# Kernel optimization log

Measured on AMD Instinct MI355X. Metric: run time of the kernel, lower is better.

## Reference

```python
import jax, jax.numpy as jnp
import numpy as np

T, N, E, F_IN, H_GNN, H_OUT, RH, G, C = 8, 10000, 160000, 128, 128, 128, 128, 32, 10


def gcn_layer(x, src, dst, W, b):
    # PyG GCNConv: h = D^-1/2 (A+I) D^-1/2 (x W) + b, self-loops added, edge weight 1
    h = x @ W  # [N, H]
    ones = jnp.ones((E,), h.dtype)
    deg = jax.ops.segment_sum(ones, dst, num_segments=N) + 1.0  # +1 for self-loop
    dinv = jax.lax.rsqrt(deg)
    coef = dinv[src] * dinv[dst]  # [E]
    agg = jax.ops.segment_sum(h[src] * coef[:, None], dst, num_segments=N)
    agg = agg + h * (dinv * dinv)[:, None]  # self-loop term
    return agg + b


def snapshot_encode(x, edge_index, batch, W1, b1, W2, b2):
    src, dst = edge_index[0], edge_index[1]
    h = jax.nn.relu(gcn_layer(x, src, dst, W1, b1))
    h = jax.nn.relu(gcn_layer(h, src, dst, W2, b2))
    sums = jax.ops.segment_sum(h, batch, num_segments=G)  # global_mean_pool
    cnts = jax.ops.segment_sum(jnp.ones((N,), h.dtype), batch, num_segments=G)
    return sums / jnp.maximum(cnts, 1.0)[:, None]  # [G, H_OUT]


def gru_layer(seq, Wih, Whh, bih, bhh):
    # seq: [T, G, in]; torch nn.GRU cell equations
    H = Whh.shape[1]

    def step(h, xt):
        gi = xt @ Wih.T + bih
        gh = h @ Whh.T + bhh
        ir, iz, inn = jnp.split(gi, 3, axis=-1)
        hr, hz, hn = jnp.split(gh, 3, axis=-1)
        r = jax.nn.sigmoid(ir + hr)
        z = jax.nn.sigmoid(iz + hz)
        n = jnp.tanh(inn + r * hn)
        h_new = (1.0 - z) * n + z * h
        return h_new, h_new

    h0 = jnp.zeros((seq.shape[1], H), seq.dtype)
    hT, outs = jax.lax.scan(step, h0, seq)
    return outs, hT


def setup_inputs() -> dict:
    key = jax.random.key(0)
    ks = jax.random.split(key, 20)
    s = 0.05
    inp = {
        "x": jax.random.normal(ks[0], (T, N, F_IN), jnp.float32),
        "edge_index": jax.random.randint(ks[1], (T, 2, E), 0, N),
        "batch": jax.random.randint(ks[2], (T, N), 0, G),
        "W1": jax.random.normal(ks[3], (F_IN, H_GNN), jnp.float32) * s,
        "b1": jnp.zeros((H_GNN,), jnp.float32),
        "W2": jax.random.normal(ks[4], (H_GNN, H_OUT), jnp.float32) * s,
        "b2": jnp.zeros((H_OUT,), jnp.float32),
        "Wih0": jax.random.normal(ks[5], (3 * RH, H_OUT), jnp.float32) * s,
        "Whh0": jax.random.normal(ks[6], (3 * RH, RH), jnp.float32) * s,
        "bih0": jnp.zeros((3 * RH,), jnp.float32),
        "bhh0": jnp.zeros((3 * RH,), jnp.float32),
        "Wih1": jax.random.normal(ks[7], (3 * RH, RH), jnp.float32) * s,
        "Whh1": jax.random.normal(ks[8], (3 * RH, RH), jnp.float32) * s,
        "bih1": jnp.zeros((3 * RH,), jnp.float32),
        "bhh1": jnp.zeros((3 * RH,), jnp.float32),
        "Wc": jax.random.normal(ks[9], (C, RH), jnp.float32) * s,
        "bc": jnp.zeros((C,), jnp.float32),
    }
    return inp


def reference(x, edge_index, batch, W1, b1, W2, b2, Wih0, Whh0, bih0, bhh0,
              Wih1, Whh1, bih1, bhh1, Wc, bc):
    # per-snapshot GNN encode, vmapped over T snapshots -> [T, G, H_OUT]
    emb = jax.vmap(snapshot_encode, in_axes=(0, 0, 0, None, None, None, None))(
        x, edge_index, batch, W1, b1, W2, b2)
    outs, _ = gru_layer(emb, Wih0, Whh0, bih0, bhh0)
    _, hT = gru_layer(outs, Wih1, Whh1, bih1, bhh1)  # h_n[-1]: last layer final state
    return hT @ Wc.T + bc  # [G, C]
```

## Files before the change

kernel.cpp:

```cpp
#include <hip/hip_runtime.h>

#define T_ 8
#define N_ 10000
#define E_ 160000
#define G_ 32
#define C_ 10
#define F_ 128

typedef _Float16 f16;
typedef _Float16 f16x2 __attribute__((ext_vector_type(2)));
typedef _Float16 f16x4 __attribute__((ext_vector_type(4)));
typedef _Float16 f16x8 __attribute__((ext_vector_type(8)));
typedef float floatx4 __attribute__((ext_vector_type(4)));

static constexpr size_t ROWS = (size_t)T_ * N_;
static constexpr int SLICE = E_ / 8;

static constexpr size_t OFF_XH    = 0;
static constexpr size_t OFF_A1    = 20480000;
static constexpr size_t OFF_H1    = 40960000;
static constexpr size_t OFF_REC   = 61440000;
static constexpr size_t OFF_CNT   = 66560000;
static constexpr size_t OFF_DINV  = 69120000;
static constexpr size_t OFF_RP    = 69440000;
static constexpr size_t OFF_CNTG  = 69760032;
static constexpr size_t OFF_BRP   = 69761056;
static constexpr size_t OFF_WP    = 69762112;
static constexpr size_t OFF_BLIST = 69827648;
static constexpr size_t OFF_GPACK = 70213184;
static constexpr size_t OFF_PART  = 70999616;

__device__ __forceinline__ float sig_fast(float x) {
  return __builtin_amdgcn_rcpf(1.0f + __builtin_amdgcn_exp2f(-1.4426950408889634f * x));
}
__device__ __forceinline__ float tanh_fast(float x) {
  return 1.0f - 2.0f * __builtin_amdgcn_rcpf(1.0f + __builtin_amdgcn_exp2f(2.8853900817779268f * x));
}

__global__ __launch_bounds__(1024) void hist_kernel(const int* __restrict__ ei,
                                                    const int* __restrict__ batch,
                                                    int* __restrict__ cnt,
                                                    int* __restrict__ cntG) {
  __shared__ int hL[N_];
  __shared__ int cL[G_];
  int b = blockIdx.x, tid = threadIdx.x;
  int t = b & 7, s = b >> 3;
  for (int i = tid; i < N_; i += 1024) hL[i] = 0;
  if (tid < G_) cL[tid] = 0;
  __syncthreads();
  const int* dstp = ei + (size_t)t * 2 * E_ + E_ + s * SLICE;
  for (int e4 = tid; e4 < SLICE / 4; e4 += 1024) {
    int4 d = *(const int4*)(dstp + e4 * 4);
    atomicAdd(&hL[d.x], 1); atomicAdd(&hL[d.y], 1);
    atomicAdd(&hL[d.z], 1); atomicAdd(&hL[d.w], 1);
  }
  if (s == 0)
    for (int n = tid; n < N_; n += 1024) atomicAdd(&cL[batch[t * N_ + n]], 1);
  __syncthreads();
  int* cp = cnt + ((size_t)t * 8 + s) * N_;
  for (int i = tid; i < N_; i += 1024) cp[i] = hL[i];
  if (s == 0 && tid < G_) cntG[t * G_ + tid] = cL[tid];
}

__global__ __launch_bounds__(1024) void scan_kernel(int* __restrict__ cnt,
                                                    int* __restrict__ rp,
                                                    float* __restrict__ dinv,
                                                    const int* __restrict__ cntG,
                                                    int* __restrict__ brp) {
  __shared__ int wsum[16];
  __shared__ int carry;
  int t = blockIdx.x, tid = threadIdx.x, lane = tid & 63, wid = tid >> 6;
  if (t == 8) {
    int v = (tid < 256) ? cntG[tid] : 0;
    for (int ofs = 1; ofs < 64; ofs <<= 1) {
      int u = __shfl_up(v, ofs);
      if (lane >= ofs) v += u;
    }
    if (lane == 63 && wid < 4) wsum[wid] = v;
    __syncthreads();
    if (tid < 256) {
      int base = 0;
      for (int w = 0; w < wid; ++w) base += wsum[w];
      if (tid == 0) brp[0] = 0;
      brp[tid + 1] = v + base;
    }
    return;
  }
  if (tid == 0) { carry = 0; rp[t * (N_ + 1)] = 0; }
  __syncthreads();
  for (int c0 = 0; c0 < N_; c0 += 1024) {
    int n = c0 + tid;
    int vs[8];
    int deg = 0;
    if (n < N_) {
#pragma unroll
      for (int s = 0; s < 8; ++s) {
        vs[s] = cnt[((size_t)t * 8 + s) * N_ + n];
        deg += vs[s];
      }
      dinv[t * N_ + n] = rsqrtf((float)deg + 1.0f);
    }
    int v = (n < N_) ? deg : 0;
    int v0 = v;
    for (int ofs = 1; ofs < 64; ofs <<= 1) {
      int u = __shfl_up(v, ofs);
      if (lane >= ofs) v += u;
    }
    if (lane == 63) wsum[wid] = v;
    __syncthreads();
    if (wid == 0) {
      int w = (lane < 16) ? wsum[lane] : 0;
      for (int ofs = 1; ofs < 16; ofs <<= 1) {
        int u = __shfl_up(w, ofs);
        if (lane >= ofs) w += u;
      }
      if (lane < 16) wsum[lane] = w;
    }
    __syncthreads();
    int base = carry + (wid ? wsum[wid - 1] : 0);
    if (n < N_) {
      rp[t * (N_ + 1) + n + 1] = base + v;
      int run = base + v - v0;
#pragma unroll
      for (int s = 0; s < 8; ++s) {
        int vv = vs[s];
        cnt[((size_t)t * 8 + s) * N_ + n] = run;
        run += vv;
      }
    }
    __syncthreads();
    if (tid == 0) carry += wsum[15];
    __syncthreads();
  }
}

__global__ __launch_bounds__(1024) void fill_kernel(const int* __restrict__ ei,
                                                    const int* __restrict__ base,
                                                    int* __restrict__ rec,
                                                    const int* __restrict__ batch,
                                                    const int* __restrict__ brp,
                                                    int* __restrict__ blist) {
  __shared__ int offL[N_];
  __shared__ int cb[G_];
  int b = blockIdx.x, tid = threadIdx.x;
  int t = b & 7, s = b >> 3;
  const int* bp = base + ((size_t)t * 8 + s) * N_;
  for (int i = tid; i < N_; i += 1024) offL[i] = bp[i];
  if (s == 0 && tid < G_) cb[tid] = brp[t * G_ + tid];
  __syncthreads();
  const int* srcp = ei + (size_t)t * 2 * E_ + s * SLICE;
  const int* dstp = srcp + E_;
  int* rt = rec + (size_t)t * E_;
  for (int e4 = tid; e4 < SLICE / 4; e4 += 1024) {
    int4 sv = *(const int4*)(srcp + e4 * 4);
    int4 dv = *(const int4*)(dstp + e4 * 4);
    int p0 = atomicAdd(&offL[dv.x], 1);
    int p1 = atomicAdd(&offL[dv.y], 1);
    int p2 = atomicAdd(&offL[dv.z], 1);
    int p3 = atomicAdd(&offL[dv.w], 1);
    rt[p0] = sv.x; rt[p1] = sv.y; rt[p2] = sv.z; rt[p3] = sv.w;
  }
  if (s == 0) {
    for (int n = tid; n < N_; n += 1024) {
      int g = batch[t * N_ + n];
      int p = atomicAdd(&cb[g], 1);
      blist[p] = t * N_ + n;
    }
  }
}

__global__ void cvt_kernel(const float* __restrict__ x, const float* __restrict__ dinv,
                           f16* __restrict__ xh) {
  size_t i = ((size_t)blockIdx.x * 256 + threadIdx.x) * 4;
  float4 v = *(const float4*)(x + i);
  float d = dinv[i >> 7];
  f16x4 o; o.x = (f16)(v.x * d); o.y = (f16)(v.y * d);
  o.z = (f16)(v.z * d); o.w = (f16)(v.w * d);
  *(f16x4*)(xh + i) = o;
}

__global__ void packall_kernel(const float* __restrict__ W1, const float* __restrict__ W2,
                               f16* __restrict__ Wp,
                               const float* __restrict__ A0, const float* __restrict__ A1,
                               const float* __restrict__ A2, const float* __restrict__ A3,
                               f16* __restrict__ gp) {
  int idx = blockIdx.x * 256 + threadIdx.x;
  if (idx < 32768) {
    const float* W = (idx < 16384) ? W1 : W2;
    int l = idx & 16383;
    int j = l & 7, lane = (l >> 3) & 63, ct = (l >> 9) & 7, kc = (l >> 12) & 3;
    int k = kc * 32 + ((lane >> 4) & 3) * 8 + j;
    int n = ct * 16 + (lane & 15);
    Wp[idx] = (f16)W[k * 128 + n];
  } else {
    int gidx = idx - 32768;
    int mat = gidx / 49152, l = gidx - mat * 49152;
    int j = l & 7, lane = (l >> 3) & 63, kc = (l >> 9) & 3, nt = l >> 11;
    int k = kc * 32 + ((lane >> 4) & 3) * 8 + j;
    int u = nt * 16 + (lane & 15);
    const float* W = (mat == 0) ? A0 : (mat == 1) ? A1 : (mat == 2) ? A2 : A3;
    gp[gidx] = (f16)W[u * 128 + k];
  }
}

template <int SCALE>
__global__ __launch_bounds__(256) void agg_gemm_kernel(
    const f16* __restrict__ X, const f16* __restrict__ Wp,
    const float* __restrict__ bias, const float* __restrict__ dinv,
    const int* __restrict__ rp, const int* __restrict__ rec,
    f16* __restrict__ O) {
  __shared__ f16x8 Bp[2048];
  __shared__ f16 At[64][136];
  int tid = threadIdx.x;
  const f16x8* Wv = (const f16x8*)Wp;
  for (int i = tid; i < 2048; i += 256) Bp[i] = Wv[i];
  __syncthreads();

  int wave = tid >> 6, lane = tid & 63;
  int b = blockIdx.x;
  int t = b & 7, chunk = b >> 3;
  int nbase = chunk * 64 + wave * 16;

  const int* rpt = rp + t * (N_ + 1);
  int rpv = 0;
  if (lane <= 16 && nbase + lane <= N_) rpv = rpt[nbase + lane];
  float dv = 0.f;
  if (lane < 16 && nbase + lane < N_) dv = dinv[t * N_ + nbase + lane];

  const f16* Xt = X + (size_t)t * N_ * F_;
  const int* rc = rec + (size_t)t * E_;

  for (int rr = 0; rr < 16; ++rr) {
    int n = nbase + rr;
    f16x2 o;
    if (n < N_) {
      int beg = __builtin_amdgcn_readfirstlane(__shfl(rpv, rr));
      int end = __builtin_amdgcn_readfirstlane(__shfl(rpv, rr + 1));
      float ds = __shfl(dv, rr);
      f16x2 xv = *(const f16x2*)(Xt + (size_t)n * F_ + 2 * lane);
      float a00 = (float)xv.x, a01 = (float)xv.y;
      float a10 = 0.f, a11 = 0.f, a20 = 0.f, a21 = 0.f, a30 = 0.f, a31 = 0.f;
      int e = beg;
      int i0 = 0, i1 = 0, i2 = 0, i3 = 0;
      if (e + 3 < end) { i0 = rc[e]; i1 = rc[e + 1]; i2 = rc[e + 2]; i3 = rc[e + 3]; }
      for (; e + 7 < end; e += 4) {
        int n0 = rc[e + 4], n1 = rc[e + 5], n2 = rc[e + 6], n3 = rc[e + 7];
        f16x2 h0 = *(const f16x2*)(Xt + (size_t)i0 * F_ + 2 * lane);
        f16x2 h1 = *(const f16x2*)(Xt + (size_t)i1 * F_ + 2 * lane);
        f16x2 h2 = *(const f16x2*)(Xt + (size_t)i2 * F_ + 2 * lane);
        f16x2 h3 = *(const f16x2*)(Xt + (size_t)i3 * F_ + 2 * lane);
        a00 += (float)h0.x; a01 += (float)h0.y;
        a10 += (float)h1.x; a11 += (float)h1.y;
        a20 += (float)h2.x; a21 += (float)h2.y;
        a30 += (float)h3.x; a31 += (float)h3.y;
        i0 = n0; i1 = n1; i2 = n2; i3 = n3;
      }
      if (e + 3 < end) {
        f16x2 h0 = *(const f16x2*)(Xt + (size_t)i0 * F_ + 2 * lane);
        f16x2 h1 = *(const f16x2*)(Xt + (size_t)i1 * F_ + 2 * lane);
        f16x2 h2 = *(const f16x2*)(Xt + (size_t)i2 * F_ + 2 * lane);
        f16x2 h3 = *(const f16x2*)(Xt + (size_t)i3 * F_ + 2 * lane);
        a00 += (float)h0.x; a01 += (float)h0.y;
        a10 += (float)h1.x; a11 += (float)h1.y;
        a20 += (float)h2.x; a21 += (float)h2.y;
        a30 += (float)h3.x; a31 += (float)h3.y;
        e += 4;
      }
      for (; e < end; ++e) {
        int s = rc[e];
        f16x2 hv = *(const f16x2*)(Xt + (size_t)s * F_ + 2 * lane);
        a00 += (float)hv.x; a01 += (float)hv.y;
      }
      float r0 = ds * ((a00 + a10) + (a20 + a30));
      float r1 = ds * ((a01 + a11) + (a21 + a31));
      o.x = (f16)r0; o.y = (f16)r1;
    } else {
      o.x = (f16)0.f; o.y = (f16)0.f;
    }
    *(f16x2*)(&At[wave * 16 + rr][2 * lane]) = o;
  }

  int quad = lane >> 4, mm = lane & 15;
  floatx4 acc[8];
#pragma unroll
  for (int ct = 0; ct < 8; ++ct) { floatx4 z = {0.f, 0.f, 0.f, 0.f}; acc[ct] = z; }
#pragma unroll
  for (int kc = 0; kc < 4; ++kc) {
    f16x8 a = *(const f16x8*)(&At[wave * 16 + mm][kc * 32 + quad * 8]);
#pragma unroll
    for (int ct = 0; ct < 8; ++ct)
      acc[ct] = __builtin_amdgcn_mfma_f32_16x16x32_f16(a, Bp[(kc * 8 + ct) * 64 + lane],
                                                       acc[ct], 0, 0, 0);
  }
  float sv[4];
#pragma unroll
  for (int r = 0; r < 4; ++r)
    sv[r] = SCALE ? __shfl(dv, quad * 4 + r) : 1.0f;
#pragma unroll
  for (int ct = 0; ct < 8; ++ct) {
    int colc = ct * 16 + mm;
    float bv = bias[colc];
#pragma unroll
    for (int r = 0; r < 4; ++r) {
      int n = nbase + quad * 4 + r;
      if (n < N_) {
        float v = fmaxf(acc[ct][r] + bv, 0.0f) * sv[r];
        O[((size_t)t * N_ + n) * F_ + colc] = (f16)v;
      }
    }
  }
}

__global__ void pool1_kernel(const f16* __restrict__ H, const int* __restrict__ brp,
                             const int* __restrict__ blist, float* __restrict__ part) {
  int b = blockIdx.x;
  int wave = threadIdx.x >> 6, lane = threadIdx.x & 63;
  int idx = b >> 1;
  int s = (b & 1) * 4 + wave;
  int beg = brp[idx], end = brp[idx + 1];
  beg = __builtin_amdgcn_readfirstlane(beg);
  end = __builtin_amdgcn_readfirstlane(end);
  int len = end - beg;
  int lo = beg + (int)(((long long)len * s) >> 3);
  int hi = beg + (int)(((long long)len * (s + 1)) >> 3);
  float a00 = 0.f, a01 = 0.f, a10 = 0.f, a11 = 0.f;
  float a20 = 0.f, a21 = 0.f, a30 = 0.f, a31 = 0.f;
  int e = lo;
  for (; e + 3 < hi; e += 4) {
    int r0 = blist[e], r1 = blist[e + 1], r2 = blist[e + 2], r3 = blist[e + 3];
    f16x2 v0 = *(const f16x2*)(H + (size_t)r0 * F_ + 2 * lane);
    f16x2 v1 = *(const f16x2*)(H + (size_t)r1 * F_ + 2 * lane);
    f16x2 v2 = *(const f16x2*)(H + (size_t)r2 * F_ + 2 * lane);
    f16x2 v3 = *(const f16x2*)(H + (size_t)r3 * F_ + 2 * lane);
    a00 += (float)v0.x; a01 += (float)v0.y;
    a10 += (float)v1.x; a11 += (float)v1.y;
    a20 += (float)v2.x; a21 += (float)v2.y;
    a30 += (float)v3.x; a31 += (float)v3.y;
  }
  for (; e < hi; ++e) {
    int r = blist[e];
    f16x2 v = *(const f16x2*)(H + (size_t)r * F_ + 2 * lane);
    a00 += (float)v.x; a01 += (float)v.y;
  }
  float2 o;
  o.x = (a00 + a10) + (a20 + a30);
  o.y = (a01 + a11) + (a21 + a31);
  *(float2*)(part + ((size_t)idx * 8 + s) * F_ + 2 * lane) = o;
}

__global__ __launch_bounds__(256, 1) void gru_mega(
    const f16* __restrict__ gp, const float* __restrict__ part,
    const int* __restrict__ brp,
    const float* __restrict__ bih0, const float* __restrict__ bhh0,
    const float* __restrict__ bih1, const float* __restrict__ bhh1,
    const float* __restrict__ Wc, const float* __restrict__ bc,
    float* __restrict__ out) {
  __shared__ f16 emb_l[16][136];
  __shared__ float gib0[16][384];
  __shared__ f16 hb0[16 * 136];
  __shared__ f16 hb1[16 * 136];
  __shared__ float ghb[2 * 384];
  __shared__ float gib[2 * 384];
  __shared__ float h1s[2 * 128];
  int tid = threadIdx.x, wave = tid >> 6, lane = tid & 63;
  int quad = lane >> 4, mm = lane & 15;
  int g2 = tid >> 7, f = tid & 127;
  int bid = blockIdx.x;

  {
    int r = tid >> 4;
    int fb = (tid & 15) * 8;
    int idx = (r >> 1) * G_ + bid * 2 + (r & 1);
    float s[8] = {0.f, 0.f, 0.f, 0.f, 0.f, 0.f, 0.f, 0.f};
#pragma unroll
    for (int k = 0; k < 8; ++k) {
      const float* p = part + ((size_t)idx * 8 + k) * F_ + fb;
      float4 v0 = *(const float4*)p;
      float4 v1 = *(const float4*)(p + 4);
      s[0] += v0.x; s[1] += v0.y; s[2] += v0.z; s[3] += v0.w;
      s[4] += v1.x; s[5] += v1.y; s[6] += v1.z; s[7] += v1.w;
    }
    float d = fmaxf((float)(brp[idx + 1] - brp[idx]), 1.0f);
    f16x8 ev;
#pragma unroll
    for (int j = 0; j < 8; ++j) ev[j] = (f16)(s[j] / d);
    *(f16x8*)(&emb_l[r][fb]) = ev;
  }
  __syncthreads();

  {
    floatx4 acc[6];
#pragma unroll
    for (int i = 0; i < 6; ++i) { floatx4 z = {0.f, 0.f, 0.f, 0.f}; acc[i] = z; }
#pragma unroll
    for (int kc = 0; kc < 4; ++kc) {
      f16x8 a = *(const f16x8*)(&emb_l[mm][kc * 32 + quad * 8]);
#pragma unroll
      for (int i = 0; i < 6; ++i) {
        int nt = wave * 6 + i;
        f16x8 bf = *(const f16x8*)(gp + (size_t)((nt * 4 + kc) * 64 + lane) * 8);
        acc[i] = __builtin_amdgcn_mfma_f32_16x16x32_f16(a, bf, acc[i], 0, 0, 0);
      }
    }
#pragma unroll
    for (int i = 0; i < 6; ++i)
#pragma unroll
      for (int r = 0; r < 4; ++r)
        gib0[quad * 4 + r][(wave * 6 + i) * 16 + mm] = acc[i][r];
  }

  f16x8 B0[24], B1[24];
#pragma unroll
  for (int i = 0; i < 6; ++i)
#pragma unroll
    for (int kc = 0; kc < 4; ++kc) {
      size_t off = (size_t)((((wave * 6 + i) * 4 + kc) * 64 + lane)) * 8;
      B0[i * 4 + kc] = *(const f16x8*)(gp + 1 * 49152 + off);
      B1[i * 4 + kc] = *(const f16x8*)(gp + 3 * 49152 + off);
    }
  float br0 = bih0[f] + bhh0[f];
  float bz0 = bih0[128 + f] + bhh0[128 + f];
  float bni0 = bih0[256 + f], bnh0 = bhh0[256 + f];
  float br1 = bih1[f] + bhh1[f];
  float bz1 = bih1[128 + f] + bhh1[128 + f];
  float bni1 = bih1[256 + f], bnh1 = bhh1[256 + f];

  for (int i = tid; i < 16 * 136; i += 256) { hb0[i] = (f16)0.f; hb1[i] = (f16)0.f; }
  float h0 = 0.f, h1 = 0.f;
  __syncthreads();

  const f16* wih1 = gp + 2 * 49152;
  for (int t = 0; t < T_; ++t) {
    f16x8 Bs[24];
#pragma unroll
    for (int i = 0; i < 6; ++i)
#pragma unroll
      for (int kc = 0; kc < 4; ++kc)
        Bs[i * 4 + kc] = *(const f16x8*)(wih1 +
            (size_t)((((wave * 6 + i) * 4 + kc) * 64 + lane)) * 8);
    const float* gi = &gib0[t * 2 + g2][0];
    float gir = gi[f], giz = gi[128 + f], gin = gi[256 + f];

    floatx4 acc[6];
#pragma unroll
    for (int i = 0; i < 6; ++i) { floatx4 z = {0.f, 0.f, 0.f, 0.f}; acc[i] = z; }
#pragma unroll
    for (int kc = 0; kc < 4; ++kc) {
      f16x8 a = *(const f16x8*)(hb0 + mm * 136 + kc * 32 + quad * 8);
#pragma unroll
      for (int i = 0; i < 6; ++i)
        acc[i] = __builtin_amdgcn_mfma_f32_16x16x32_f16(a, B0[i * 4 + kc], acc[i], 0, 0, 0);
    }
    if (quad == 0) {
#pragma unroll
      for (int i = 0; i < 6; ++i) {
        ghb[0 * 384 + wave * 96 + i * 16 + mm] = acc[i][0];
        ghb[1 * 384 + wave * 96 + i * 16 + mm] = acc[i][1];
      }
    }
    __syncthreads();

    {
      float hr = ghb[g2 * 384 + f];
      float hz = ghb[g2 * 384 + 128 + f];
      float hn = ghb[g2 * 384 + 256 + f];
      float r = sig_fast(gir + hr + br0);
      float z = sig_fast(giz + hz + bz0);
      float nn = tanh_fast(gin + bni0 + r * (hn + bnh0));
      h0 = (1.0f - z) * nn + z * h0;
      hb0[g2 * 136 + f] = (f16)h0;
    }
    __syncthreads();

    floatx4 accx[6], acch[6];
#pragma unroll
    for (int i = 0; i < 6; ++i) {
      floatx4 z = {0.f, 0.f, 0.f, 0.f}; accx[i] = z; acch[i] = z;
    }
#pragma unroll
    for (int kc = 0; kc < 4; ++kc) {
      f16x8 ax = *(const f16x8*)(hb0 + mm * 136 + kc * 32 + quad * 8);
      f16x8 ah = *(const f16x8*)(hb1 + mm * 136 + kc * 32 + quad * 8);
#pragma unroll
      for (int i = 0; i < 6; ++i) {
        accx[i] = __builtin_amdgcn_mfma_f32_16x16x32_f16(ax, Bs[i * 4 + kc], accx[i], 0, 0, 0);
        acch[i] = __builtin_amdgcn_mfma_f32_16x16x32_f16(ah, B1[i * 4 + kc], acch[i], 0, 0, 0);
      }
    }
    if (quad == 0) {
#pragma unroll
      for (int i = 0; i < 6; ++i) {
        gib[0 * 384 + wave * 96 + i * 16 + mm] = accx[i][0];
        gib[1 * 384 + wave * 96 + i * 16 + mm] = accx[i][1];
        ghb[0 * 384 + wave * 96 + i * 16 + mm] = acch[i][0];
        ghb[1 * 384 + wave * 96 + i * 16 + mm] = acch[i][1];
      }
    }
    __syncthreads();

    {
      float i1r = gib[g2 * 384 + f];
      float i1z = gib[g2 * 384 + 128 + f];
      float i1n = gib[g2 * 384 + 256 + f];
      float hr = ghb[g2 * 384 + f];
      float hz = ghb[g2 * 384 + 128 + f];
      float hn = ghb[g2 * 384 + 256 + f];
      float r = sig_fast(i1r + hr + br1);
      float z = sig_fast(i1z + hz + bz1);
      float nn = tanh_fast(i1n + bni1 + r * (hn + bnh1));
      h1 = (1.0f - z) * nn + z * h1;
      hb1[g2 * 136 + f] = (f16)h1;
    }
    __syncthreads();
  }

  h1s[g2 * 128 + f] = h1;
  __syncthreads();
  if (tid < 2 * C_) {
    int gg = tid / C_, c = tid - gg * C_;
    float s = bc[c];
    const float* wr = Wc + (size_t)c * 128;
    const float* hr = h1s + gg * 128;
    for (int k = 0; k < 128; k += 4) {
      float4 w = *(const float4*)(wr + k);
      s += hr[k] * w.x + hr[k + 1] * w.y + hr[k + 2] * w.z + hr[k + 3] * w.w;
    }
    out[(bid * 2 + gg) * C_ + c] = s;
  }
}

extern "C" void kernel_launch(void* const* d_in, const int* in_sizes, int n_in,
                              void* d_out, int out_size, void* d_ws, size_t ws_size,
                              hipStream_t stream) {
  const float* x    = (const float*)d_in[0];
  const int*   ei   = (const int*)d_in[1];
  const int*   batch= (const int*)d_in[2];
  const float* W1   = (const float*)d_in[3];
  const float* b1   = (const float*)d_in[4];
  const float* W2   = (const float*)d_in[5];
  const float* b2   = (const float*)d_in[6];
  const float* Wih0 = (const float*)d_in[7];
  const float* Whh0 = (const float*)d_in[8];
  const float* bih0 = (const float*)d_in[9];
  const float* bhh0 = (const float*)d_in[10];
  const float* Wih1 = (const float*)d_in[11];
  const float* Whh1 = (const float*)d_in[12];
  const float* bih1 = (const float*)d_in[13];
  const float* bhh1 = (const float*)d_in[14];
  const float* Wc   = (const float*)d_in[15];
  const float* bc   = (const float*)d_in[16];
  float* out = (float*)d_out;

  char* ws = (char*)d_ws;
  f16*   Xh    = (f16*)(ws + OFF_XH);
  f16*   H1    = (f16*)(ws + OFF_H1);
  f16*   H2    = Xh;
  int*   rec   = (int*)(ws + OFF_REC);
  int*   cnt   = (int*)(ws + OFF_CNT);
  float* dinv  = (float*)(ws + OFF_DINV);
  int*   rp    = (int*)(ws + OFF_RP);
  int*   cntG  = (int*)(ws + OFF_CNTG);
  int*   brp   = (int*)(ws + OFF_BRP);
  f16*   Wp    = (f16*)(ws + OFF_WP);
  int*   blist = (int*)(ws + OFF_BLIST);
  f16*   gp    = (f16*)(ws + OFF_GPACK);
  float* part  = (float*)(ws + OFF_PART);

  packall_kernel<<<896, 256, 0, stream>>>(W1, W2, Wp, Wih0, Whh0, Wih1, Whh1, gp);
  hist_kernel<<<64, 1024, 0, stream>>>(ei, batch, cnt, cntG);
  scan_kernel<<<9, 1024, 0, stream>>>(cnt, rp, dinv, cntG, brp);
  cvt_kernel<<<10000, 256, 0, stream>>>(x, dinv, Xh);
  fill_kernel<<<64, 1024, 0, stream>>>(ei, cnt, rec, batch, brp, blist);

  agg_gemm_kernel<1><<<8 * 157, 256, 0, stream>>>(Xh, Wp, b1, dinv, rp, rec, H1);
  agg_gemm_kernel<0><<<8 * 157, 256, 0, stream>>>(H1, Wp + 16384, b2, dinv, rp, rec, H2);

  pool1_kernel<<<512, 256, 0, stream>>>(H2, brp, blist, part);
  gru_mega<<<16, 256, 0, stream>>>(gp, part, brp, bih0, bhh0, bih1, bhh1, Wc, bc, out);
}
```

Before: 344.0 us.

## Split fused aggregate-GEMM into separate gather-aggregate and MFMA GEMM kernels

Replaces the fused kernel, which had each wave aggregate 16 nodes in sequence with f16x2 loads per lane, with a standalone aggregation kernel. The new kernel gives each wave one node and splits the edges across four lane groups that each do 16-byte f16x8 gathers, then reduces the groups with cross-lane shuffles. A separate MFMA GEMM kernel reads the aggregated rows straight from global memory. The aim is more memory-level parallelism and better load balance for the irregular gather. The cost is an extra round trip through global memory for the intermediate buffer and two more kernel launches per forward pass.

Result: faster. 297.8 us (-13.4%).

```diff
diff --git a/kernel.cpp b/kernel.cpp
--- a/kernel.cpp
+++ b/kernel.cpp
@@ -177,6 +177,67 @@
   f16x4 o; o.x = (f16)(v.x * d); o.y = (f16)(v.y * d);
   o.z = (f16)(v.z * d); o.w = (f16)(v.w * d);
   *(f16x4*)(xh + i) = o;
+}
+
+__global__ __launch_bounds__(256) void agg_kernel(const f16* __restrict__ X, f16* __restrict__ A,
+                                                  const int* __restrict__ rp,
+                                                  const int* __restrict__ rec,
+                                                  const float* __restrict__ dinv) {
+  int wave = threadIdx.x >> 6, lane = threadIdx.x & 63;
+  int eg = lane >> 4;
+  int cb = (lane & 15) * 8;
+  int b = blockIdx.x;
+  int t = b & 7, i = b >> 3;
+  int n = i * 4 + wave;
+  int row = t * N_ + n;
+  float ds = dinv[row];
+  int beg = rp[t * (N_ + 1) + n], end = rp[t * (N_ + 1) + n + 1];
+  beg = __builtin_amdgcn_readfirstlane(beg);
+  end = __builtin_amdgcn_readfirstlane(end);
+  const int* rc = rec + (size_t)t * E_;
+  const f16* Xt = X + (size_t)t * N_ * F_;
+
+  float s[8] = {0.f, 0.f, 0.f, 0.f, 0.f, 0.f, 0.f, 0.f};
+  if (eg == 3) {
+    f16x8 v = *(const f16x8*)(Xt + (size_t)n * F_ + cb);
+#pragma unroll
+    for (int j = 0; j < 8; ++j) s[j] += (float)v[j];
+  }
+  int cnt = end - beg;
+  int nq = cnt >> 2;
+  int e = beg + eg;
+  if (nq > 0) {
+    int rid = rc[e];
+    for (int q = 0; q + 1 < nq; ++q) {
+      int nrid = rc[e + 4];
+      f16x8 v = *(const f16x8*)(Xt + (size_t)rid * F_ + cb);
+#pragma unroll
+      for (int j = 0; j < 8; ++j) s[j] += (float)v[j];
+      rid = nrid; e += 4;
+    }
+    f16x8 v = *(const f16x8*)(Xt + (size_t)rid * F_ + cb);
+#pragma unroll
+    for (int j = 0; j < 8; ++j) s[j] += (float)v[j];
+    e += 4;
+  }
+  int rem = cnt & 3;
+  if (eg < rem) {
+    int rid = rc[e];
+    f16x8 v = *(const f16x8*)(Xt + (size_t)rid * F_ + cb);
+#pragma unroll
+    for (int j = 0; j < 8; ++j) s[j] += (float)v[j];
+  }
+#pragma unroll
+  for (int j = 0; j < 8; ++j) {
+    s[j] += __shfl_xor(s[j], 16);
+    s[j] += __shfl_xor(s[j], 32);
+  }
+  if (eg == 0) {
+    f16x8 o;
+#pragma unroll
+    for (int j = 0; j < 8; ++j) o[j] = (f16)(ds * s[j]);
+    *(f16x8*)(A + (size_t)row * F_ + cb) = o;
+  }
 }
 
 __global__ void packall_kernel(const float* __restrict__ W1, const float* __restrict__ W2,
@@ -203,90 +264,25 @@
   }
 }
 
-template <int SCALE>
-__global__ __launch_bounds__(256) void agg_gemm_kernel(
-    const f16* __restrict__ X, const f16* __restrict__ Wp,
-    const float* __restrict__ bias, const float* __restrict__ dinv,
-    const int* __restrict__ rp, const int* __restrict__ rec,
-    f16* __restrict__ O) {
+__global__ __launch_bounds__(256) void gemm_kernel(const f16* __restrict__ A,
+                                                   const f16* __restrict__ Wp,
+                                                   const float* __restrict__ bias,
+                                                   const float* __restrict__ scale,
+                                                   f16* __restrict__ O) {
   __shared__ f16x8 Bp[2048];
-  __shared__ f16 At[64][136];
-  int tid = threadIdx.x;
   const f16x8* Wv = (const f16x8*)Wp;
-  for (int i = tid; i < 2048; i += 256) Bp[i] = Wv[i];
-  __syncthreads();
-
-  int wave = tid >> 6, lane = tid & 63;
-  int b = blockIdx.x;
-  int t = b & 7, chunk = b >> 3;
-  int nbase = chunk * 64 + wave * 16;
-
-  const int* rpt = rp + t * (N_ + 1);
-  int rpv = 0;
-  if (lane <= 16 && nbase + lane <= N_) rpv = rpt[nbase + lane];
-  float dv = 0.f;
-  if (lane < 16 && nbase + lane < N_) dv = dinv[t * N_ + nbase + lane];
-
-  const f16* Xt = X + (size_t)t * N_ * F_;
-  const int* rc = rec + (size_t)t * E_;
-
-  for (int rr = 0; rr < 16; ++rr) {
-    int n = nbase + rr;
-    f16x2 o;
-    if (n < N_) {
-      int beg = __builtin_amdgcn_readfirstlane(__shfl(rpv, rr));
-      int end = __builtin_amdgcn_readfirstlane(__shfl(rpv, rr + 1));
-      float ds = __shfl(dv, rr);
-      f16x2 xv = *(const f16x2*)(Xt + (size_t)n * F_ + 2 * lane);
-      float a00 = (float)xv.x, a01 = (float)xv.y;
-      float a10 = 0.f, a11 = 0.f, a20 = 0.f, a21 = 0.f, a30 = 0.f, a31 = 0.f;
-      int e = beg;
-      int i0 = 0, i1 = 0, i2 = 0, i3 = 0;
-      if (e + 3 < end) { i0 = rc[e]; i1 = rc[e + 1]; i2 = rc[e + 2]; i3 = rc[e + 3]; }
-      for (; e + 7 < end; e += 4) {
-        int n0 = rc[e + 4], n1 = rc[e + 5], n2 = rc[e + 6], n3 = rc[e + 7];
-        f16x2 h0 = *(const f16x2*)(Xt + (size_t)i0 * F_ + 2 * lane);
-        f16x2 h1 = *(const f16x2*)(Xt + (size_t)i1 * F_ + 2 * lane);
-        f16x2 h2 = *(const f16x2*)(Xt + (size_t)i2 * F_ + 2 * lane);
-        f16x2 h3 = *(const f16x2*)(Xt + (size_t)i3 * F_ + 2 * lane);
-        a00 += (float)h0.x; a01 += (float)h0.y;
-        a10 += (float)h1.x; a11 += (float)h1.y;
-        a20 += (float)h2.x; a21 += (float)h2.y;
-        a30 += (float)h3.x; a31 += (float)h3.y;
-        i0 = n0; i1 = n1; i2 = n2; i3 = n3;
-      }
-      if (e + 3 < end) {
-        f16x2 h0 = *(const f16x2*)(Xt + (size_t)i0 * F_ + 2 * lane);
-        f16x2 h1 = *(const f16x2*)(Xt + (size_t)i1 * F_ + 2 * lane);
-        f16x2 h2 = *(const f16x2*)(Xt + (size_t)i2 * F_ + 2 * lane);
-        f16x2 h3 = *(const f16x2*)(Xt + (size_t)i3 * F_ + 2 * lane);
-        a00 += (float)h0.x; a01 += (float)h0.y;
-        a10 += (float)h1.x; a11 += (float)h1.y;
-        a20 += (float)h2.x; a21 += (float)h2.y;
-        a30 += (float)h3.x; a31 += (float)h3.y;
-        e += 4;
-      }
-      for (; e < end; ++e) {
-        int s = rc[e];
-        f16x2 hv = *(const f16x2*)(Xt + (size_t)s * F_ + 2 * lane);
-        a00 += (float)hv.x; a01 += (float)hv.y;
-      }
-      float r0 = ds * ((a00 + a10) + (a20 + a30));
-      float r1 = ds * ((a01 + a11) + (a21 + a31));
-      o.x = (f16)r0; o.y = (f16)r1;
-    } else {
-      o.x = (f16)0.f; o.y = (f16)0.f;
-    }
-    *(f16x2*)(&At[wave * 16 + rr][2 * lane]) = o;
-  }
-
-  int quad = lane >> 4, mm = lane & 15;
+  for (int i = threadIdx.x; i < 2048; i += 256) Bp[i] = Wv[i];
+  __syncthreads();
+  int wave = threadIdx.x >> 6, lane = threadIdx.x & 63;
+  int quad = lane >> 4, m = lane & 15;
+  int rowbase = blockIdx.x * 64 + wave * 16;
+  const f16x8* Arow = (const f16x8*)(A + (size_t)(rowbase + m) * F_);
   floatx4 acc[8];
 #pragma unroll
   for (int ct = 0; ct < 8; ++ct) { floatx4 z = {0.f, 0.f, 0.f, 0.f}; acc[ct] = z; }
 #pragma unroll
   for (int kc = 0; kc < 4; ++kc) {
-    f16x8 a = *(const f16x8*)(&At[wave * 16 + mm][kc * 32 + quad * 8]);
+    f16x8 a = Arow[kc * 4 + quad];
 #pragma unroll
     for (int ct = 0; ct < 8; ++ct)
       acc[ct] = __builtin_amdgcn_mfma_f32_16x16x32_f16(a, Bp[(kc * 8 + ct) * 64 + lane],
@@ -295,18 +291,16 @@
   float sv[4];
 #pragma unroll
   for (int r = 0; r < 4; ++r)
-    sv[r] = SCALE ? __shfl(dv, quad * 4 + r) : 1.0f;
+    sv[r] = scale ? scale[rowbase + quad * 4 + r] : 1.0f;
 #pragma unroll
   for (int ct = 0; ct < 8; ++ct) {
-    int colc = ct * 16 + mm;
+    int colc = ct * 16 + m;
     float bv = bias[colc];
 #pragma unroll
     for (int r = 0; r < 4; ++r) {
-      int n = nbase + quad * 4 + r;
-      if (n < N_) {
-        float v = fmaxf(acc[ct][r] + bv, 0.0f) * sv[r];
-        O[((size_t)t * N_ + n) * F_ + colc] = (f16)v;
-      }
+      int row = rowbase + quad * 4 + r;
+      float v = fmaxf(acc[ct][r] + bv, 0.0f) * sv[r];
+      O[(size_t)row * F_ + colc] = (f16)v;
     }
   }
 }
@@ -553,7 +547,9 @@
 
   char* ws = (char*)d_ws;
   f16*   Xh    = (f16*)(ws + OFF_XH);
+  f16*   A1    = (f16*)(ws + OFF_A1);
   f16*   H1    = (f16*)(ws + OFF_H1);
+  f16*   A2    = A1;
   f16*   H2    = Xh;
   int*   rec   = (int*)(ws + OFF_REC);
   int*   cnt   = (int*)(ws + OFF_CNT);
@@ -572,8 +568,10 @@
   cvt_kernel<<<10000, 256, 0, stream>>>(x, dinv, Xh);
   fill_kernel<<<64, 1024, 0, stream>>>(ei, cnt, rec, batch, brp, blist);
 
-  agg_gemm_kernel<1><<<8 * 157, 256, 0, stream>>>(Xh, Wp, b1, dinv, rp, rec, H1);
-  agg_gemm_kernel<0><<<8 * 157, 256, 0, stream>>>(H1, Wp + 16384, b2, dinv, rp, rec, H2);
+  agg_kernel<<<20000, 256, 0, stream>>>(Xh, A1, rp, rec, dinv);
+  gemm_kernel<<<1250, 256, 0, stream>>>(A1, Wp, b1, dinv, H1);
+  agg_kernel<<<20000, 256, 0, stream>>>(H1, A2, rp, rec, dinv);
+  gemm_kernel<<<1250, 256, 0, stream>>>(A2, Wp + 16384, b2, (const float*)nullptr, H2);
 
   pool1_kernel<<<512, 256, 0, stream>>>(H2, brp, blist, part);
   gru_mega<<<16, 256, 0, stream>>>(gp, part, brp, bih0, bhh0, bih1, bhh1, Wc, bc, out);
```
